# Optimization experiments

Measured on AMD Instinct MI355X. Metric: run time of the kernel, lower is better.

## Reference

```python
import jax, jax.numpy as jnp
import numpy as np

B, OBS, T, H, A = 16384, 256, 16, 512, 16


def setup_inputs() -> dict:
    key = jax.random.key(0)
    ks = jax.random.split(key, 10)
    s0 = 1.0 / np.sqrt(OBS)
    s1 = 1.0 / np.sqrt(H)
    return {
        "x": jax.random.normal(ks[0], (B, OBS), jnp.float32),
        "task_ids": jax.random.randint(ks[1], (B,), 0, T),
        # actor stacked per-task weights
        "aW0": jax.random.normal(ks[2], (T, OBS, H), jnp.float32) * s0,
        "ab0": jnp.zeros((T, H), jnp.float32),
        "aW1": jax.random.normal(ks[3], (T, H, H), jnp.float32) * s1,
        "ab1": jnp.zeros((T, H), jnp.float32),
        "aW2": jax.random.normal(ks[4], (T, H, A), jnp.float32) * 0.01,
        "ab2": jnp.zeros((T, A), jnp.float32),
        # critic stacked per-task weights
        "cW0": jax.random.normal(ks[5], (T, OBS, H), jnp.float32) * s0,
        "cb0": jnp.zeros((T, H), jnp.float32),
        "cW1": jax.random.normal(ks[6], (T, H, H), jnp.float32) * s1,
        "cb1": jnp.zeros((T, H), jnp.float32),
        "cW2": jax.random.normal(ks[7], (T, H, 1), jnp.float32) * s1,
        "cb2": jnp.zeros((T, 1), jnp.float32),
    }


def _all_task_mlp(x, W0, b0, W1, b1, W2, b2):
    # Densely evaluate all T per-task MLPs on the full batch (faithful to the
    # original vmap + Python-loop-over-tasks pattern, vectorized as batched GEMMs).
    h = jnp.tanh(jnp.einsum('bi,tio->bto', x, W0) + b0)        # [B,T,H]
    h = jnp.tanh(jnp.einsum('bti,tio->bto', h, W1) + b1)       # [B,T,H]
    return jnp.einsum('bti,tio->bto', h, W2) + b2              # [B,T,out]


def reference(x, task_ids, aW0, ab0, aW1, ab1, aW2, ab2,
              cW0, cb0, cW1, cb1, cW2, cb2):
    actor_out = _all_task_mlp(x, aW0, ab0, aW1, ab1, aW2, ab2)   # [B,T,A]
    critic_out = _all_task_mlp(x, cW0, cb0, cW1, cb1, cW2, cb2)  # [B,T,1]
    one_hot = jnp.eye(T, dtype=x.dtype)[task_ids]                # [B,T]
    logits = jnp.einsum('bto,bt->bo', actor_out, one_hot)        # [B,A]
    values = jnp.einsum('bto,bt->bo', critic_out, one_hot)[:, 0] # [B]
    return logits, values
```

## Files before the change

kernel.cpp:

```cpp
#include <hip/hip_runtime.h>

#define B_N   16384
#define OBS_N 256
#define T_N   16
#define H_N   512
#define A_N   16

typedef __attribute__((ext_vector_type(8))) short  bf16x8;
typedef __attribute__((ext_vector_type(4))) float  f32x4;

#define IDX_OFF   1024
#define W_PK_OFF  (2u * 1024u * 1024u)
#define PK_A0     0
#define PK_A1     262144
#define PK_C0     786432
#define PK_C1     1048576
#define PK_TASK   1572864
#define WS_NEED   ((size_t)W_PK_OFF + (size_t)T_N * PK_TASK * 2u)

__device__ __forceinline__ unsigned short f2bf(float x) {
    unsigned u = __float_as_uint(x);
    u += 0x7FFFu + ((u >> 16) & 1u);
    return (unsigned short)(u >> 16);
}
__device__ __forceinline__ float bf2f(unsigned short h) {
    return __uint_as_float(((unsigned)h) << 16);
}
__device__ __forceinline__ float tanh_fast(float v) {
    return 1.0f - 2.0f / (__expf(2.0f * v) + 1.0f);
}

__global__ void bin_kernel(const int* __restrict__ task_ids,
                           int* __restrict__ counts,
                           int* __restrict__ idx)
{
    int b = blockIdx.x * blockDim.x + threadIdx.x;
    if (b < B_N) {
        int t = task_ids[b];
        int p = atomicAdd(&counts[t], 1);
        idx[t * B_N + p] = b;
    }
}

__global__ __launch_bounds__(256)
void conv_pack(const float* __restrict__ aW0, const float* __restrict__ aW1,
               const float* __restrict__ cW0, const float* __restrict__ cW1,
               unsigned short* __restrict__ wp)
{
    __shared__ float sf[32 * 512];
    const int bid = blockIdx.x;
    const int t = bid / 48, s = bid % 48;
    const float* src; int K, ks, pk;
    if (s < 8)       { src = aW0; K = 256; ks = s;      pk = PK_A0; }
    else if (s < 24) { src = aW1; K = 512; ks = s - 8;  pk = PK_A1; }
    else if (s < 32) { src = cW0; K = 256; ks = s - 24; pk = PK_C0; }
    else             { src = cW1; K = 512; ks = s - 32; pk = PK_C1; }

    const int tid = threadIdx.x;
    const float* sp = src + ((size_t)t * K + (size_t)ks * 32) * 512;
    #pragma unroll
    for (int i = 0; i < 16; ++i) {
        int f = tid + i * 256;
        *(float4*)(sf + f * 4) = *(const float4*)(sp + f * 4);
    }
    __syncthreads();

    unsigned short* wt = wp + (size_t)t * PK_TASK + pk;
    const int KS = K / 32;
    #pragma unroll
    for (int u = 0; u < 8; ++u) {
        int p    = u * 256 + tid;
        int nt   = p >> 6;
        int lane = p & 63;
        int ln   = lane & 15;
        int ko   = (lane >> 4) * 8;
        unsigned hi2[4], lo2[4];
        #pragma unroll
        for (int jj = 0; jj < 4; ++jj) {
            float v0 = sf[(ko + 2 * jj + 0) * 512 + nt * 16 + ln];
            float v1 = sf[(ko + 2 * jj + 1) * 512 + nt * 16 + ln];
            unsigned short h0 = f2bf(v0), h1 = f2bf(v1);
            unsigned short l0 = f2bf(v0 - bf2f(h0));
            unsigned short l1 = f2bf(v1 - bf2f(h1));
            hi2[jj] = (unsigned)h0 | ((unsigned)h1 << 16);
            lo2[jj] = (unsigned)l0 | ((unsigned)l1 << 16);
        }
        size_t base = (size_t)(nt * KS + ks) * 1024 + lane * 8;
        *(uint4*)(wt + base)       = make_uint4(hi2[0], hi2[1], hi2[2], hi2[3]);
        *(uint4*)(wt + base + 512) = make_uint4(lo2[0], lo2[1], lo2[2], lo2[3]);
    }
}

template <int K, bool LO>
__device__ __forceinline__ void gemm_pass(const unsigned short* __restrict__ wseg,
                                          const char* __restrict__ ahb,
                                          const char* __restrict__ alb,
                                          int w, int lane, f32x4 acc[4][4])
{
    constexpr int KS = K / 32;
    const int ln  = lane & 15;
    const int lk  = (lane >> 4) * 8;
    const int swz = (ln & 7) << 4;
    const unsigned short* bp = wseg + (size_t)(w * 4) * KS * 1024 + lane * 8
                                    + (LO ? 512 : 0);
    int abase[4];
    #pragma unroll
    for (int m = 0; m < 4; ++m)
        abase[m] = ((m * 16 + ln) * K + lk) * 2;

    bf16x8 b0 = *(const bf16x8*)(bp);
    bf16x8 b1 = *(const bf16x8*)(bp + (size_t)KS * 1024);
    #pragma unroll 1
    for (int s = 0; s < KS; ++s) {
        bf16x8 ah[4], al[4];
        #pragma unroll
        for (int m = 0; m < 4; ++m) {
            int ab = (abase[m] + s * 64) ^ swz;
            ah[m] = *(const bf16x8*)(ahb + ab);
        }
        if (!LO) {
            #pragma unroll
            for (int m = 0; m < 4; ++m) {
                int ab = (abase[m] + s * 64) ^ swz;
                al[m] = *(const bf16x8*)(alb + ab);
            }
        }
        #pragma unroll
        for (int ct = 0; ct < 4; ++ct) {
            int pct = ct + 2, ps = s;
            if (pct >= 4) { pct -= 4; ps = s + 1; }
            if (ps >= KS) { pct = 3; ps = KS - 1; }
            bf16x8 b2 = *(const bf16x8*)(bp + (size_t)(pct * KS + ps) * 1024);
            #pragma unroll
            for (int m = 0; m < 4; ++m)
                acc[m][ct] = __builtin_amdgcn_mfma_f32_16x16x32_bf16(ah[m], b0, acc[m][ct], 0, 0, 0);
            if (!LO) {
                #pragma unroll
                for (int m = 0; m < 4; ++m)
                    acc[m][ct] = __builtin_amdgcn_mfma_f32_16x16x32_bf16(al[m], b0, acc[m][ct], 0, 0, 0);
            }
            b0 = b1; b1 = b2;
        }
    }
}

__device__ __forceinline__ void zero_acc(f32x4 acc[4][4]) {
#pragma unroll
    for (int m = 0; m < 4; ++m)
#pragma unroll
        for (int ct = 0; ct < 4; ++ct)
            acc[m][ct] = (f32x4){0.f, 0.f, 0.f, 0.f};
}

__device__ __forceinline__ void epi_tanh(f32x4 acc[4][4], const float* __restrict__ bias,
                                         char* ahb, char* alb, int w, int lane)
{
    const int q4 = (lane >> 4) * 4;
    const int ln = lane & 15;
#pragma unroll
    for (int ct = 0; ct < 4; ++ct) {
        int col = w * 64 + ct * 16 + ln;
        float b = bias[col];
#pragma unroll
        for (int m = 0; m < 4; ++m) {
#pragma unroll
            for (int q = 0; q < 4; ++q) {
                int row = m * 16 + q4 + q;
                float t = tanh_fast(acc[m][ct][q] + b);
                unsigned short h = f2bf(t);
                unsigned short l = f2bf(t - bf2f(h));
                int byte = ((row * 512 + col) * 2) ^ ((row & 7) << 4);
                *(unsigned short*)(ahb + byte) = h;
                *(unsigned short*)(alb + byte) = l;
            }
        }
    }
}

__device__ __forceinline__ void epi_h2(f32x4 acc[4][4], const float* __restrict__ bias,
                                       char* h2b, int w, int lane)
{
    const int q4 = (lane >> 4) * 4;
    const int ln = lane & 15;
#pragma unroll
    for (int ct = 0; ct < 4; ++ct) {
        int col = w * 64 + ct * 16 + ln;
        float b = bias[col];
#pragma unroll
        for (int m = 0; m < 4; ++m) {
#pragma unroll
            for (int q = 0; q < 4; ++q) {
                int row = m * 16 + q4 + q;
                float t = tanh_fast(acc[m][ct][q] + b);
                int byte = (row * 2048 + col * 4) ^ ((row & 7) << 4);
                *(float*)(h2b + byte) = t;
            }
        }
    }
}

__device__ __forceinline__ void gather_xs(const float* __restrict__ x,
                                          const int* __restrict__ tidx_lds, int nrows,
                                          char* xhb, char* xlb, int tid)
{
#pragma unroll
    for (int kk = 0; kk < 8; ++kk) {
        int f   = tid + kk * 512;
        int row = f >> 6;
        int c4  = f & 63;
        int rr  = min(row, nrows - 1);
        int sid = tidx_lds[rr];
        float4 v = *(const float4*)(x + (size_t)sid * OBS_N + c4 * 4);
        unsigned short h0 = f2bf(v.x), h1 = f2bf(v.y), h2e = f2bf(v.z), h3 = f2bf(v.w);
        unsigned short l0 = f2bf(v.x - bf2f(h0)), l1 = f2bf(v.y - bf2f(h1));
        unsigned short l2 = f2bf(v.z - bf2f(h2e)), l3 = f2bf(v.w - bf2f(h3));
        uint2 hp = make_uint2((unsigned)h0 | ((unsigned)h1 << 16), (unsigned)h2e | ((unsigned)h3 << 16));
        uint2 lp = make_uint2((unsigned)l0 | ((unsigned)l1 << 16), (unsigned)l2 | ((unsigned)l3 << 16));
        int byte = ((row * OBS_N + c4 * 4) * 2) ^ ((row & 7) << 4);
        *(uint2*)(xhb + byte) = hp;
        *(uint2*)(xlb + byte) = lp;
    }
}

__device__ __forceinline__ void actor_head(const char* __restrict__ h2b,
                                           const float* __restrict__ W2,
                                           const float* __restrict__ b2,
                                           const int* __restrict__ tidx_lds, int nrows,
                                           float* __restrict__ out, int tid)
{
#pragma unroll
    for (int oo = 0; oo < 2; ++oo) {
        int o = tid + oo * 512;
        int r = o >> 4, a = o & 15;
        float acc = 0.f;
#pragma unroll 4
        for (int i = 0; i < H_N; i += 4) {
            int byte = (r * 2048 + i * 4) ^ ((r & 7) << 4);
            float4 hv = *(const float4*)(h2b + byte);
            acc = fmaf(hv.x, W2[(i + 0) * A_N + a], acc);
            acc = fmaf(hv.y, W2[(i + 1) * A_N + a], acc);
            acc = fmaf(hv.z, W2[(i + 2) * A_N + a], acc);
            acc = fmaf(hv.w, W2[(i + 3) * A_N + a], acc);
        }
        if (r < nrows)
            out[(size_t)tidx_lds[r] * A_N + a] = acc + b2[a];
    }
}

__device__ __forceinline__ void critic_head(const char* __restrict__ h2b,
                                            const float* __restrict__ W2, float b2,
                                            const int* __restrict__ tidx_lds, int nrows,
                                            float* __restrict__ out, int tid)
{
    int r = tid >> 3, sub = tid & 7;
    float acc = 0.f;
#pragma unroll
    for (int j = 0; j < 16; ++j) {
        int i = sub * 4 + j * 32;
        int byte = (r * 2048 + i * 4) ^ ((r & 7) << 4);
        float4 hv = *(const float4*)(h2b + byte);
        float4 wv = *(const float4*)(W2 + i);
        acc = fmaf(hv.x, wv.x, acc);
        acc = fmaf(hv.y, wv.y, acc);
        acc = fmaf(hv.z, wv.z, acc);
        acc = fmaf(hv.w, wv.w, acc);
    }
    acc += __shfl_xor(acc, 1);
    acc += __shfl_xor(acc, 2);
    acc += __shfl_xor(acc, 4);
    if (sub == 0 && r < nrows)
        out[B_N * A_N + tidx_lds[r]] = acc + b2;
}

__global__ __launch_bounds__(512, 2)
void moe_mfma_kernel(const float* __restrict__ x,
                     const int* __restrict__ counts,
                     const int* __restrict__ idx,
                     const unsigned short* __restrict__ wp,
                     const float* __restrict__ ab0, const float* __restrict__ ab1,
                     const float* __restrict__ aW2, const float* __restrict__ ab2,
                     const float* __restrict__ cb0, const float* __restrict__ cb1,
                     const float* __restrict__ cW2, const float* __restrict__ cb2,
                     float* __restrict__ out)
{
    extern __shared__ char lds[];
    char* lo_half  = lds + 65536;
    int*  tidx_lds = (int*)(lds + 131072);

    const int bx   = blockIdx.x;
    const int task = bx & 15;
    const int slot = bx >> 4;
    const int cnt  = counts[task];
    const int tid  = threadIdx.x;
    const int w    = tid >> 6;
    const int lane = tid & 63;

    const unsigned short* wt = wp + (size_t)task * PK_TASK;

    for (int r0 = slot * 64; r0 < cnt; r0 += 1024) {
        int nrows = min(64, cnt - r0);

        __syncthreads();
        if (tid < 64) {
            int rr = min(tid, nrows - 1);
            tidx_lds[tid] = idx[task * B_N + r0 + rr];
        }
        __syncthreads();

        f32x4 acc[4][4];

        gather_xs(x, tidx_lds, nrows, lds, lo_half, tid);
        __syncthreads();
        zero_acc(acc);
        gemm_pass<256, false>(wt + PK_A0, lds, lo_half, w, lane, acc);
        gemm_pass<256, true >(wt + PK_A0, lds, lo_half, w, lane, acc);
        __syncthreads();
        epi_tanh(acc, ab0 + task * H_N, lds, lo_half, w, lane);
        __syncthreads();
        zero_acc(acc);
        gemm_pass<512, false>(wt + PK_A1, lds, lo_half, w, lane, acc);
        gemm_pass<512, true >(wt + PK_A1, lds, lo_half, w, lane, acc);
        __syncthreads();
        epi_h2(acc, ab1 + task * H_N, lds, w, lane);
        __syncthreads();
        actor_head(lds, aW2 + (size_t)task * H_N * A_N, ab2 + task * A_N,
                   tidx_lds, nrows, out, tid);
        __syncthreads();

        gather_xs(x, tidx_lds, nrows, lds, lo_half, tid);
        __syncthreads();
        zero_acc(acc);
        gemm_pass<256, false>(wt + PK_C0, lds, lo_half, w, lane, acc);
        gemm_pass<256, true >(wt + PK_C0, lds, lo_half, w, lane, acc);
        __syncthreads();
        epi_tanh(acc, cb0 + task * H_N, lds, lo_half, w, lane);
        __syncthreads();
        zero_acc(acc);
        gemm_pass<512, false>(wt + PK_C1, lds, lo_half, w, lane, acc);
        gemm_pass<512, true >(wt + PK_C1, lds, lo_half, w, lane, acc);
        __syncthreads();
        epi_h2(acc, cb1 + task * H_N, lds, w, lane);
        __syncthreads();
        critic_head(lds, cW2 + (size_t)task * H_N, cb2[task],
                    tidx_lds, nrows, out, tid);
    }
}

#define ROWS 16
template <int IN, bool TANH>
__device__ __forceinline__ void layer_block(const float* __restrict__ in_lds,
                                            const float* __restrict__ W,
                                            const float* __restrict__ bias,
                                            float* __restrict__ out_lds,
                                            int w, int lane)
{
#pragma unroll
    for (int cgi = 0; cgi < 2; ++cgi) {
        const int c = (w + 4 * cgi) * 64 + lane;
        float acc[ROWS];
#pragma unroll
        for (int r = 0; r < ROWS; ++r) acc[r] = 0.0f;
        const float* Wc = W + c;
#pragma unroll 2
        for (int i = 0; i < IN; i += 4) {
            float w0 = Wc[(i + 0) * H_N];
            float w1 = Wc[(i + 1) * H_N];
            float w2 = Wc[(i + 2) * H_N];
            float w3 = Wc[(i + 3) * H_N];
#pragma unroll
            for (int r = 0; r < ROWS; ++r) {
                float4 xv = *reinterpret_cast<const float4*>(&in_lds[r * IN + i]);
                acc[r] = fmaf(xv.x, w0, acc[r]);
                acc[r] = fmaf(xv.y, w1, acc[r]);
                acc[r] = fmaf(xv.z, w2, acc[r]);
                acc[r] = fmaf(xv.w, w3, acc[r]);
            }
        }
        float bb = bias[c];
#pragma unroll
        for (int r = 0; r < ROWS; ++r) {
            float v = acc[r] + bb;
            if (TANH) v = 1.0f - 2.0f / (__expf(2.0f * v) + 1.0f);
            out_lds[r * H_N + c] = v;
        }
    }
}

__global__ __launch_bounds__(256, 2)
void mlp_fallback(const float* __restrict__ x,
                  const int* __restrict__ counts,
                  const int* __restrict__ idx,
                  const float* __restrict__ aW0, const float* __restrict__ ab0,
                  const float* __restrict__ aW1, const float* __restrict__ ab1,
                  const float* __restrict__ aW2, const float* __restrict__ ab2,
                  const float* __restrict__ cW0, const float* __restrict__ cb0,
                  const float* __restrict__ cW1, const float* __restrict__ cb1,
                  const float* __restrict__ cW2, const float* __restrict__ cb2,
                  float* __restrict__ out)
{
    extern __shared__ float flds[];
    float* xs  = flds;
    float* hb0 = flds + ROWS * OBS_N;
    float* hb1 = hb0 + ROWS * H_N;

    const int bx    = blockIdx.x;
    const int phase = bx >> 11;
    const int task  = (bx & 7) + (phase << 3);
    const int tile  = (bx >> 3) & 255;
    const int cnt   = counts[task];
    const int r0    = tile * ROWS;
    if (r0 >= cnt) return;
    const int nrows = min(ROWS, cnt - r0);
    const int tid   = threadIdx.x;
    const int lane  = tid & 63;
    const int w     = tid >> 6;
    const int* tidx = idx + task * B_N + r0;

    {
        const float4* x4  = reinterpret_cast<const float4*>(x);
        float4*       xs4 = reinterpret_cast<float4*>(xs);
#pragma unroll
        for (int k = 0; k < 4; ++k) {
            int f = tid + k * 256;
            int r = f >> 6, c4 = f & 63;
            int rr = (r < nrows) ? r : (nrows - 1);
            xs4[f] = x4[(size_t)tidx[rr] * (OBS_N / 4) + c4];
        }
    }
    __syncthreads();
    layer_block<OBS_N, true>(xs,  aW0 + task * OBS_N * H_N, ab0 + task * H_N, hb0, w, lane);
    __syncthreads();
    layer_block<H_N,  true>(hb0, aW1 + task * H_N * H_N,   ab1 + task * H_N, hb1, w, lane);
    __syncthreads();
    {
        const float* W2 = aW2 + task * H_N * A_N;
        const float* b2 = ab2 + task * A_N;
        int r = tid >> 4, a = tid & 15;
        float acc = 0.0f;
#pragma unroll 4
        for (int i = 0; i < H_N; i += 4) {
            float4 hv = *reinterpret_cast<const float4*>(&hb1[r * H_N + i]);
            acc = fmaf(hv.x, W2[(i + 0) * A_N + a], acc);
            acc = fmaf(hv.y, W2[(i + 1) * A_N + a], acc);
            acc = fmaf(hv.z, W2[(i + 2) * A_N + a], acc);
            acc = fmaf(hv.w, W2[(i + 3) * A_N + a], acc);
        }
        acc += b2[a];
        if (r < nrows) out[(size_t)tidx[r] * A_N + a] = acc;
    }
    layer_block<OBS_N, true>(xs, cW0 + task * OBS_N * H_N, cb0 + task * H_N, hb0, w, lane);
    __syncthreads();
    layer_block<H_N,  true>(hb0, cW1 + task * H_N * H_N,  cb1 + task * H_N, hb1, w, lane);
    __syncthreads();
    {
        const float* W2 = cW2 + task * H_N;
        const float  b2 = cb2[task];
        int r = tid >> 4, sub = tid & 15;
        float acc = 0.0f;
#pragma unroll
        for (int k = 0; k < 32; k += 4) {
            int i = sub * 32 + k;
            float4 hv = *reinterpret_cast<const float4*>(&hb1[r * H_N + i]);
            float4 wv = *reinterpret_cast<const float4*>(&W2[i]);
            acc = fmaf(hv.x, wv.x, acc);
            acc = fmaf(hv.y, wv.y, acc);
            acc = fmaf(hv.z, wv.z, acc);
            acc = fmaf(hv.w, wv.w, acc);
        }
        acc += __shfl_xor(acc, 1);
        acc += __shfl_xor(acc, 2);
        acc += __shfl_xor(acc, 4);
        acc += __shfl_xor(acc, 8);
        if (sub == 0 && r < nrows) out[B_N * A_N + tidx[r]] = acc + b2;
    }
}

extern "C" void kernel_launch(void* const* d_in, const int* in_sizes, int n_in,
                              void* d_out, int out_size, void* d_ws, size_t ws_size,
                              hipStream_t stream)
{
    const float* x        = (const float*)d_in[0];
    const int*   task_ids = (const int*)  d_in[1];
    const float* aW0 = (const float*)d_in[2];
    const float* ab0 = (const float*)d_in[3];
    const float* aW1 = (const float*)d_in[4];
    const float* ab1 = (const float*)d_in[5];
    const float* aW2 = (const float*)d_in[6];
    const float* ab2 = (const float*)d_in[7];
    const float* cW0 = (const float*)d_in[8];
    const float* cb0 = (const float*)d_in[9];
    const float* cW1 = (const float*)d_in[10];
    const float* cb1 = (const float*)d_in[11];
    const float* cW2 = (const float*)d_in[12];
    const float* cb2 = (const float*)d_in[13];
    float* out = (float*)d_out;

    int* counts = (int*)d_ws;
    int* idx    = (int*)((char*)d_ws + IDX_OFF);

    hipMemsetAsync(counts, 0, T_N * sizeof(int), stream);
    bin_kernel<<<B_N / 256, 256, 0, stream>>>(task_ids, counts, idx);

    if (ws_size >= WS_NEED) {
        unsigned short* wpk = (unsigned short*)((char*)d_ws + W_PK_OFF);
        conv_pack<<<T_N * 48, 256, 0, stream>>>(aW0, aW1, cW0, cW1, wpk);
        moe_mfma_kernel<<<256, 512, 131584, stream>>>(
            x, counts, idx, wpk,
            ab0, ab1, aW2, ab2, cb0, cb1, cW2, cb2, out);
    } else {
        size_t lds_bytes = (size_t)(ROWS * OBS_N + 2 * ROWS * H_N) * sizeof(float);
        mlp_fallback<<<2 * 8 * 256, 256, lds_bytes, stream>>>(
            x, counts, idx,
            aW0, ab0, aW1, ab1, aW2, ab2,
            cW0, cb0, cW1, cb1, cW2, cb2, out);
    }
}
```

Measured before the change: 696.0 us.

## Restructure grouped MLP kernel to 32-row tiles with fused split-bf16 GEMM passes

Shrinks the row tile from 64 to 32 and fuses the hi and lo GEMM passes into one loop issuing three MFMAs (hi*hi, lo*hi, hi*lo) per step. Weight fragments for the next k-step are prefetched from global into registers. LDS is split into separate regions so gathered x is loaded once and reused by actor and critic, with fewer barriers. Block-to-task mapping changes to 8 XCD groups, each processing two tasks. The intent is to cut redundant gathers, syncs and weight-fragment re-reads, at the cost of more LDS per block (160 KB, which may drop occupancy to one block per CU) and more weight traffic per row.

```diff
diff --git a/kernel.cpp b/kernel.cpp
--- a/kernel.cpp
+++ b/kernel.cpp
@@ -91,69 +91,68 @@
     }
 }
 
-template <int K, bool LO>
-__device__ __forceinline__ void gemm_pass(const unsigned short* __restrict__ wseg,
-                                          const char* __restrict__ ahb,
-                                          const char* __restrict__ alb,
-                                          int w, int lane, f32x4 acc[4][4])
+template <int K>
+__device__ __forceinline__ void gemm32(const unsigned short* __restrict__ wseg,
+                                       const char* __restrict__ ahb,
+                                       const char* __restrict__ alb,
+                                       int w, int lane, f32x4 acc[2][4])
 {
     constexpr int KS = K / 32;
     const int ln  = lane & 15;
     const int lk  = (lane >> 4) * 8;
     const int swz = (ln & 7) << 4;
-    const unsigned short* bp = wseg + (size_t)(w * 4) * KS * 1024 + lane * 8
-                                    + (LO ? 512 : 0);
-    int abase[4];
+    const unsigned short* bp = wseg + (size_t)(w * 4) * KS * 1024 + lane * 8;
+    int abase[2];
+    abase[0] = (ln * K + lk) * 2;
+    abase[1] = ((16 + ln) * K + lk) * 2;
+
+    bf16x8 bh[4], bl[4], nh[4], nl[4];
     #pragma unroll
-    for (int m = 0; m < 4; ++m)
-        abase[m] = ((m * 16 + ln) * K + lk) * 2;
-
-    bf16x8 b0 = *(const bf16x8*)(bp);
-    bf16x8 b1 = *(const bf16x8*)(bp + (size_t)KS * 1024);
+    for (int ct = 0; ct < 4; ++ct) {
+        const unsigned short* q = bp + (size_t)(ct * KS) * 1024;
+        bh[ct] = *(const bf16x8*)q;
+        bl[ct] = *(const bf16x8*)(q + 512);
+    }
     #pragma unroll 1
     for (int s = 0; s < KS; ++s) {
-        bf16x8 ah[4], al[4];
+        const int sp = (s + 1 < KS) ? s + 1 : s;
         #pragma unroll
-        for (int m = 0; m < 4; ++m) {
+        for (int ct = 0; ct < 4; ++ct) {
+            const unsigned short* q = bp + (size_t)(ct * KS + sp) * 1024;
+            nh[ct] = *(const bf16x8*)q;
+            nl[ct] = *(const bf16x8*)(q + 512);
+        }
+        bf16x8 ah[2], al[2];
+        #pragma unroll
+        for (int m = 0; m < 2; ++m) {
             int ab = (abase[m] + s * 64) ^ swz;
             ah[m] = *(const bf16x8*)(ahb + ab);
-        }
-        if (!LO) {
+            al[m] = *(const bf16x8*)(alb + ab);
+        }
+        #pragma unroll
+        for (int m = 0; m < 2; ++m) {
             #pragma unroll
-            for (int m = 0; m < 4; ++m) {
-                int ab = (abase[m] + s * 64) ^ swz;
-                al[m] = *(const bf16x8*)(alb + ab);
+            for (int ct = 0; ct < 4; ++ct) {
+                acc[m][ct] = __builtin_amdgcn_mfma_f32_16x16x32_bf16(ah[m], bh[ct], acc[m][ct], 0, 0, 0);
+                acc[m][ct] = __builtin_amdgcn_mfma_f32_16x16x32_bf16(al[m], bh[ct], acc[m][ct], 0, 0, 0);
+                acc[m][ct] = __builtin_amdgcn_mfma_f32_16x16x32_bf16(ah[m], bl[ct], acc[m][ct], 0, 0, 0);
             }
         }
         #pragma unroll
-        for (int ct = 0; ct < 4; ++ct) {
-            int pct = ct + 2, ps = s;
-            if (pct >= 4) { pct -= 4; ps = s + 1; }
-            if (ps >= KS) { pct = 3; ps = KS - 1; }
-            bf16x8 b2 = *(const bf16x8*)(bp + (size_t)(pct * KS + ps) * 1024);
-            #pragma unroll
-            for (int m = 0; m < 4; ++m)
-                acc[m][ct] = __builtin_amdgcn_mfma_f32_16x16x32_bf16(ah[m], b0, acc[m][ct], 0, 0, 0);
-            if (!LO) {
-                #pragma unroll
-                for (int m = 0; m < 4; ++m)
-                    acc[m][ct] = __builtin_amdgcn_mfma_f32_16x16x32_bf16(al[m], b0, acc[m][ct], 0, 0, 0);
-            }
-            b0 = b1; b1 = b2;
-        }
-    }
-}
-
-__device__ __forceinline__ void zero_acc(f32x4 acc[4][4]) {
-#pragma unroll
-    for (int m = 0; m < 4; ++m)
+        for (int ct = 0; ct < 4; ++ct) { bh[ct] = nh[ct]; bl[ct] = nl[ct]; }
+    }
+}
+
+__device__ __forceinline__ void zero_acc(f32x4 acc[2][4]) {
+#pragma unroll
+    for (int m = 0; m < 2; ++m)
 #pragma unroll
         for (int ct = 0; ct < 4; ++ct)
             acc[m][ct] = (f32x4){0.f, 0.f, 0.f, 0.f};
 }
 
-__device__ __forceinline__ void epi_tanh(f32x4 acc[4][4], const float* __restrict__ bias,
-                                         char* ahb, char* alb, int w, int lane)
+__device__ __forceinline__ void epi_tanh(f32x4 acc[2][4], const float* __restrict__ bias,
+                                         char* hhb, char* hlb, int w, int lane)
 {
     const int q4 = (lane >> 4) * 4;
     const int ln = lane & 15;
@@ -162,7 +161,7 @@
         int col = w * 64 + ct * 16 + ln;
         float b = bias[col];
 #pragma unroll
-        for (int m = 0; m < 4; ++m) {
+        for (int m = 0; m < 2; ++m) {
 #pragma unroll
             for (int q = 0; q < 4; ++q) {
                 int row = m * 16 + q4 + q;
@@ -170,14 +169,14 @@
                 unsigned short h = f2bf(t);
                 unsigned short l = f2bf(t - bf2f(h));
                 int byte = ((row * 512 + col) * 2) ^ ((row & 7) << 4);
-                *(unsigned short*)(ahb + byte) = h;
-                *(unsigned short*)(alb + byte) = l;
-            }
-        }
-    }
-}
-
-__device__ __forceinline__ void epi_h2(f32x4 acc[4][4], const float* __restrict__ bias,
+                *(unsigned short*)(hhb + byte) = h;
+                *(unsigned short*)(hlb + byte) = l;
+            }
+        }
+    }
+}
+
+__device__ __forceinline__ void epi_h2(f32x4 acc[2][4], const float* __restrict__ bias,
                                        char* h2b, int w, int lane)
 {
     const int q4 = (lane >> 4) * 4;
@@ -187,7 +186,7 @@
         int col = w * 64 + ct * 16 + ln;
         float b = bias[col];
 #pragma unroll
-        for (int m = 0; m < 4; ++m) {
+        for (int m = 0; m < 2; ++m) {
 #pragma unroll
             for (int q = 0; q < 4; ++q) {
                 int row = m * 16 + q4 + q;
@@ -199,150 +198,118 @@
     }
 }
 
-__device__ __forceinline__ void gather_xs(const float* __restrict__ x,
-                                          const int* __restrict__ tidx_lds, int nrows,
-                                          char* xhb, char* xlb, int tid)
-{
-#pragma unroll
-    for (int kk = 0; kk < 8; ++kk) {
-        int f   = tid + kk * 512;
-        int row = f >> 6;
-        int c4  = f & 63;
-        int rr  = min(row, nrows - 1);
-        int sid = tidx_lds[rr];
-        float4 v = *(const float4*)(x + (size_t)sid * OBS_N + c4 * 4);
-        unsigned short h0 = f2bf(v.x), h1 = f2bf(v.y), h2e = f2bf(v.z), h3 = f2bf(v.w);
-        unsigned short l0 = f2bf(v.x - bf2f(h0)), l1 = f2bf(v.y - bf2f(h1));
-        unsigned short l2 = f2bf(v.z - bf2f(h2e)), l3 = f2bf(v.w - bf2f(h3));
-        uint2 hp = make_uint2((unsigned)h0 | ((unsigned)h1 << 16), (unsigned)h2e | ((unsigned)h3 << 16));
-        uint2 lp = make_uint2((unsigned)l0 | ((unsigned)l1 << 16), (unsigned)l2 | ((unsigned)l3 << 16));
-        int byte = ((row * OBS_N + c4 * 4) * 2) ^ ((row & 7) << 4);
-        *(uint2*)(xhb + byte) = hp;
-        *(uint2*)(xlb + byte) = lp;
-    }
-}
-
-__device__ __forceinline__ void actor_head(const char* __restrict__ h2b,
-                                           const float* __restrict__ W2,
-                                           const float* __restrict__ b2,
-                                           const int* __restrict__ tidx_lds, int nrows,
-                                           float* __restrict__ out, int tid)
-{
-#pragma unroll
-    for (int oo = 0; oo < 2; ++oo) {
-        int o = tid + oo * 512;
-        int r = o >> 4, a = o & 15;
-        float acc = 0.f;
-#pragma unroll 4
-        for (int i = 0; i < H_N; i += 4) {
-            int byte = (r * 2048 + i * 4) ^ ((r & 7) << 4);
-            float4 hv = *(const float4*)(h2b + byte);
-            acc = fmaf(hv.x, W2[(i + 0) * A_N + a], acc);
-            acc = fmaf(hv.y, W2[(i + 1) * A_N + a], acc);
-            acc = fmaf(hv.z, W2[(i + 2) * A_N + a], acc);
-            acc = fmaf(hv.w, W2[(i + 3) * A_N + a], acc);
-        }
-        if (r < nrows)
-            out[(size_t)tidx_lds[r] * A_N + a] = acc + b2[a];
-    }
-}
-
-__device__ __forceinline__ void critic_head(const char* __restrict__ h2b,
-                                            const float* __restrict__ W2, float b2,
-                                            const int* __restrict__ tidx_lds, int nrows,
-                                            float* __restrict__ out, int tid)
-{
-    int r = tid >> 3, sub = tid & 7;
-    float acc = 0.f;
-#pragma unroll
-    for (int j = 0; j < 16; ++j) {
-        int i = sub * 4 + j * 32;
-        int byte = (r * 2048 + i * 4) ^ ((r & 7) << 4);
-        float4 hv = *(const float4*)(h2b + byte);
-        float4 wv = *(const float4*)(W2 + i);
-        acc = fmaf(hv.x, wv.x, acc);
-        acc = fmaf(hv.y, wv.y, acc);
-        acc = fmaf(hv.z, wv.z, acc);
-        acc = fmaf(hv.w, wv.w, acc);
-    }
-    acc += __shfl_xor(acc, 1);
-    acc += __shfl_xor(acc, 2);
-    acc += __shfl_xor(acc, 4);
-    if (sub == 0 && r < nrows)
-        out[B_N * A_N + tidx_lds[r]] = acc + b2;
-}
-
 __global__ __launch_bounds__(512, 2)
-void moe_mfma_kernel(const float* __restrict__ x,
-                     const int* __restrict__ counts,
-                     const int* __restrict__ idx,
-                     const unsigned short* __restrict__ wp,
-                     const float* __restrict__ ab0, const float* __restrict__ ab1,
-                     const float* __restrict__ aW2, const float* __restrict__ ab2,
-                     const float* __restrict__ cb0, const float* __restrict__ cb1,
-                     const float* __restrict__ cW2, const float* __restrict__ cb2,
-                     float* __restrict__ out)
+void moe_mfma32(const float* __restrict__ x,
+                const int* __restrict__ counts,
+                const int* __restrict__ idx,
+                const unsigned short* __restrict__ wp,
+                const float* __restrict__ ab0, const float* __restrict__ ab1,
+                const float* __restrict__ aW2, const float* __restrict__ ab2,
+                const float* __restrict__ cb0, const float* __restrict__ cb1,
+                const float* __restrict__ cW2, const float* __restrict__ cb2,
+                float* __restrict__ out)
 {
     extern __shared__ char lds[];
-    char* lo_half  = lds + 65536;
-    int*  tidx_lds = (int*)(lds + 131072);
+    char* xs_hi = lds;
+    char* xs_lo = lds + 16384;
+    char* h_hi  = lds + 32768;
+    char* h_lo  = lds + 65536;
+    char* h2b   = lds + 98304;
 
     const int bx   = blockIdx.x;
-    const int task = bx & 15;
-    const int slot = bx >> 4;
-    const int cnt  = counts[task];
+    const int xcd  = bx & 7;
+    const int slot = bx >> 3;
     const int tid  = threadIdx.x;
     const int w    = tid >> 6;
     const int lane = tid & 63;
 
-    const unsigned short* wt = wp + (size_t)task * PK_TASK;
-
-    for (int r0 = slot * 64; r0 < cnt; r0 += 1024) {
-        int nrows = min(64, cnt - r0);
-
-        __syncthreads();
-        if (tid < 64) {
-            int rr = min(tid, nrows - 1);
-            tidx_lds[tid] = idx[task * B_N + r0 + rr];
-        }
-        __syncthreads();
-
-        f32x4 acc[4][4];
-
-        gather_xs(x, tidx_lds, nrows, lds, lo_half, tid);
-        __syncthreads();
-        zero_acc(acc);
-        gemm_pass<256, false>(wt + PK_A0, lds, lo_half, w, lane, acc);
-        gemm_pass<256, true >(wt + PK_A0, lds, lo_half, w, lane, acc);
-        __syncthreads();
-        epi_tanh(acc, ab0 + task * H_N, lds, lo_half, w, lane);
-        __syncthreads();
-        zero_acc(acc);
-        gemm_pass<512, false>(wt + PK_A1, lds, lo_half, w, lane, acc);
-        gemm_pass<512, true >(wt + PK_A1, lds, lo_half, w, lane, acc);
-        __syncthreads();
-        epi_h2(acc, ab1 + task * H_N, lds, w, lane);
-        __syncthreads();
-        actor_head(lds, aW2 + (size_t)task * H_N * A_N, ab2 + task * A_N,
-                   tidx_lds, nrows, out, tid);
-        __syncthreads();
-
-        gather_xs(x, tidx_lds, nrows, lds, lo_half, tid);
-        __syncthreads();
-        zero_acc(acc);
-        gemm_pass<256, false>(wt + PK_C0, lds, lo_half, w, lane, acc);
-        gemm_pass<256, true >(wt + PK_C0, lds, lo_half, w, lane, acc);
-        __syncthreads();
-        epi_tanh(acc, cb0 + task * H_N, lds, lo_half, w, lane);
-        __syncthreads();
-        zero_acc(acc);
-        gemm_pass<512, false>(wt + PK_C1, lds, lo_half, w, lane, acc);
-        gemm_pass<512, true >(wt + PK_C1, lds, lo_half, w, lane, acc);
-        __syncthreads();
-        epi_h2(acc, cb1 + task * H_N, lds, w, lane);
-        __syncthreads();
-        critic_head(lds, cW2 + (size_t)task * H_N, cb2[task],
-                    tidx_lds, nrows, out, tid);
+    #pragma unroll 1
+    for (int p = 0; p < 2; ++p) {
+        const int task = xcd + 8 * p;
+        const int cnt  = counts[task];
+        const unsigned short* wt  = wp + (size_t)task * PK_TASK;
+        const int*            tix = idx + task * B_N;
+
+        #pragma unroll 1
+        for (int r0 = slot * 32; r0 < cnt; r0 += 1024) {
+            const int nrows = min(32, cnt - r0);
+
+            #pragma unroll
+            for (int k = 0; k < 4; ++k) {
+                int f   = tid + k * 512;
+                int row = f >> 6;
+                int c4  = f & 63;
+                int sid = tix[r0 + min(row, nrows - 1)];
+                float4 v = *(const float4*)(x + (size_t)sid * OBS_N + c4 * 4);
+                unsigned short e0 = f2bf(v.x), e1 = f2bf(v.y), e2 = f2bf(v.z), e3 = f2bf(v.w);
+                unsigned short g0 = f2bf(v.x - bf2f(e0)), g1 = f2bf(v.y - bf2f(e1));
+                unsigned short g2 = f2bf(v.z - bf2f(e2)), g3 = f2bf(v.w - bf2f(e3));
+                uint2 hp = make_uint2((unsigned)e0 | ((unsigned)e1 << 16), (unsigned)e2 | ((unsigned)e3 << 16));
+                uint2 lp = make_uint2((unsigned)g0 | ((unsigned)g1 << 16), (unsigned)g2 | ((unsigned)g3 << 16));
+                int byte = ((row * OBS_N + c4 * 4) * 2) ^ ((row & 7) << 4);
+                *(uint2*)(xs_hi + byte) = hp;
+                *(uint2*)(xs_lo + byte) = lp;
+            }
+            __syncthreads();
+
+            f32x4 acc[2][4];
+
+            zero_acc(acc);
+            gemm32<256>(wt + PK_A0, xs_hi, xs_lo, w, lane, acc);
+            epi_tanh(acc, ab0 + task * H_N, h_hi, h_lo, w, lane);
+            __syncthreads();
+            zero_acc(acc);
+            gemm32<512>(wt + PK_A1, h_hi, h_lo, w, lane, acc);
+            epi_h2(acc, ab1 + task * H_N, h2b, w, lane);
+            __syncthreads();
+            {
+                const float* W2 = aW2 + (size_t)task * H_N * A_N;
+                int r = tid >> 4, a = tid & 15;
+                float s = 0.f;
+                #pragma unroll 4
+                for (int i = 0; i < H_N; i += 4) {
+                    int byte = (r * 2048 + i * 4) ^ ((r & 7) << 4);
+                    float4 hv = *(const float4*)(h2b + byte);
+                    s = fmaf(hv.x, W2[(i + 0) * A_N + a], s);
+                    s = fmaf(hv.y, W2[(i + 1) * A_N + a], s);
+                    s = fmaf(hv.z, W2[(i + 2) * A_N + a], s);
+                    s = fmaf(hv.w, W2[(i + 3) * A_N + a], s);
+                }
+                if (r < nrows)
+                    out[(size_t)tix[r0 + r] * A_N + a] = s + ab2[task * A_N + a];
+            }
+
+            zero_acc(acc);
+            gemm32<256>(wt + PK_C0, xs_hi, xs_lo, w, lane, acc);
+            epi_tanh(acc, cb0 + task * H_N, h_hi, h_lo, w, lane);
+            __syncthreads();
+            zero_acc(acc);
+            gemm32<512>(wt + PK_C1, h_hi, h_lo, w, lane, acc);
+            epi_h2(acc, cb1 + task * H_N, h2b, w, lane);
+            __syncthreads();
+            {
+                const float* W2 = cW2 + (size_t)task * H_N;
+                int r = tid >> 4, sub = tid & 15;
+                float s = 0.f;
+                #pragma unroll
+                for (int j = 0; j < 8; ++j) {
+                    int i = j * 64 + sub * 4;
+                    int byte = (r * 2048 + i * 4) ^ ((r & 7) << 4);
+                    float4 hv = *(const float4*)(h2b + byte);
+                    float4 wv = *(const float4*)(W2 + i);
+                    s = fmaf(hv.x, wv.x, s);
+                    s = fmaf(hv.y, wv.y, s);
+                    s = fmaf(hv.z, wv.z, s);
+                    s = fmaf(hv.w, wv.w, s);
+                }
+                s += __shfl_xor(s, 1);
+                s += __shfl_xor(s, 2);
+                s += __shfl_xor(s, 4);
+                s += __shfl_xor(s, 8);
+                if (sub == 0 && r < nrows)
+                    out[B_N * A_N + tix[r0 + r]] = s + cb2[task];
+            }
+        }
     }
 }
 
@@ -504,7 +471,7 @@
     if (ws_size >= WS_NEED) {
         unsigned short* wpk = (unsigned short*)((char*)d_ws + W_PK_OFF);
         conv_pack<<<T_N * 48, 256, 0, stream>>>(aW0, aW1, cW0, cW1, wpk);
-        moe_mfma_kernel<<<256, 512, 131584, stream>>>(
+        moe_mfma32<<<256, 512, 163840, stream>>>(
             x, counts, idx, wpk,
             ab0, ab1, aW2, ab2, cb0, cb1, cW2, cb2, out);
     } else {
```

Result: faster. 639.2 us (-8.2%).
